# Optimization experiments

Hardware: AMD Instinct MI355X
Metric: run time of the kernel (lower is better)

The kernel has to match this reference:

```python
import jax, jax.numpy as jnp
import numpy as np

RATIO = 2
KSIZE = 12
PAD = KSIZE // 2 - RATIO // 2  # 5


def setup_inputs() -> dict:
    key = jax.random.key(0)
    k1, k2 = jax.random.split(key)
    x = jax.random.normal(k1, (4, 64, 256, 256), dtype=jnp.float32)
    # fixed anti-aliasing filter buffer (kaiser-jinc in original); random stand-in
    filt = jax.random.normal(k2, (KSIZE, KSIZE), dtype=jnp.float32)
    return {"x": x, "filt": filt}


def reference(x, filt):
    B, C, H, W = x.shape
    # reflect pad
    xp = jnp.pad(x, ((0, 0), (0, 0), (PAD, PAD), (PAD, PAD)), mode="reflect")
    # depthwise conv_transpose2d(stride=RATIO, groups=C) == conv with
    # lhs_dilation=RATIO, full padding (k-1), spatially flipped kernel
    w = jnp.broadcast_to(filt[::-1, ::-1][None, None], (C, 1, KSIZE, KSIZE))
    y = jax.lax.conv_general_dilated(
        xp, w,
        window_strides=(1, 1),
        padding=[(KSIZE - 1, KSIZE - 1)] * 2,
        lhs_dilation=(RATIO, RATIO),
        dimension_numbers=("NCHW", "OIHW", "NCHW"),
        feature_group_count=C,
    )
    y = (RATIO ** 2) * y
    pl = PAD * RATIO + (KSIZE - RATIO) // 2       # 15
    pr = PAD * RATIO + (KSIZE - RATIO + 1) // 2   # 15
    return y[..., pl:-pr, pl:-pr]
```

## Files before the change

### kernel.cpp

```cpp
#include <hip/hip_runtime.h>


#define S 40
#define TW 1552

typedef float v2f __attribute__((ext_vector_type(2)));
typedef __attribute__((address_space(3))) void lds_t;
typedef __attribute__((address_space(1))) const void gm_t;

__global__ void filter_prep(const float* __restrict__ filt, float* __restrict__ ws)
{
    int t = threadIdx.x;
    if (t < 144) {
        int n = t % 6, m = (t / 6) % 6, px = (t / 36) & 1, py = t / 72;
        float f = 4.0f * filt[(11 - py - 2 * m) * 12 + (11 - px - 2 * n)];
        ws[2 * t]     = f;
        ws[2 * t + 1] = f;
    }
}

__global__ __launch_bounds__(256, 4) void upsample2d_kernel(
    const float* __restrict__ x, const v2f* __restrict__ ftp,
    float* __restrict__ out)
{
    __shared__ float s_in[2 * TW];

    const int tx = threadIdx.x, ty = threadIdx.y;
    const int w    = ty >> 2;
    const int lane = (ty & 3) * 16 + tx;
    const int bc0 = blockIdx.z;
    const int boy = blockIdx.y, box = blockIdx.x;

    int goff[6];
    #pragma unroll
    for (int k = 0; k < 6; ++k) {
        int j = w * 384 + 64 * k + lane;
        if (j > 1519) j = 1519;
        int r = (j * 1639) >> 16;
        int c = j - r * 40;
        int gy = boy * 32 - 3 + r, gx = box * 32 - 3 + c;
        gy = gy < 0 ? -gy : gy;  gy = gy > 255 ? 510 - gy : gy;
        gx = gx < 0 ? -gx : gx;  gx = gx > 255 ? 510 - gx : gx;
        goff[k] = gy * 256 + gx;
    }

    const float* x0 = x + (size_t)bc0 * 65536;
    const float* x1 = x0 + (size_t)128 * 65536;

    #pragma unroll
    for (int k = 0; k < 6; ++k)
        __builtin_amdgcn_global_load_lds((gm_t*)(x0 + goff[k]),
                                         (lds_t*)(s_in + w * 384 + 64 * k), 4, 0, 0);
    #pragma unroll
    for (int k = 0; k < 6; ++k)
        __builtin_amdgcn_global_load_lds((gm_t*)(x1 + goff[k]),
                                         (lds_t*)(s_in + TW + w * 384 + 64 * k), 4, 0, 0);

    const int xb  = (2 * ty) * S + 2 * tx;
    const int OY0 = boy * 64 + 4 * ty;
    const int OX  = box * 64 + 4 * tx;

    auto tile = [&](const int sbase, float* oc) {
        v2f accp[4][2] = {};
        #pragma unroll
        for (int r = 0; r < 8; ++r) {
            const int rb = sbase + xb + r * S;
            v2f e[4], o[3];
            #pragma unroll
            for (int j = 0; j < 4; ++j)
                e[j] = *reinterpret_cast<const v2f*>(&s_in[rb + 2 * j]);
            #pragma unroll
            for (int j = 0; j < 3; ++j) {
                o[j].x = s_in[rb + 2 * j + 1];
                o[j].y = s_in[rb + 2 * j + 2];
            }
            #pragma unroll
            for (int qy = 0; qy < 2; ++qy)
            #pragma unroll
            for (int py = 0; py < 2; ++py) {
                const int m = r - qy - py;
                if (m >= 0 && m <= 5) {
                    #pragma unroll
                    for (int px = 0; px < 2; ++px)
                    #pragma unroll
                    for (int n = 0; n < 6; ++n) {
                        const int c = px + n;
                        const v2f xp = (c & 1) ? o[(c - 1) >> 1] : e[c >> 1];
                        const v2f f2 = ftp[((py * 2 + px) * 6 + m) * 6 + n];
                        accp[2 * qy + py][px] =
                            __builtin_elementwise_fma(xp, f2, accp[2 * qy + py][px]);
                    }
                }
            }
        }
        #pragma unroll
        for (int oy = 0; oy < 4; ++oy) {
            float4 v = make_float4(accp[oy][0].x, accp[oy][1].x,
                                   accp[oy][0].y, accp[oy][1].y);
            *reinterpret_cast<float4*>(&oc[(size_t)(OY0 + oy) * 512 + OX]) = v;
        }
    };

    asm volatile("s_waitcnt vmcnt(6)" ::: "memory");
    __builtin_amdgcn_sched_barrier(0);
    __builtin_amdgcn_s_barrier();
    __builtin_amdgcn_sched_barrier(0);
    tile(0, out + (size_t)bc0 * 262144);

    asm volatile("s_waitcnt vmcnt(16)" ::: "memory");
    __builtin_amdgcn_sched_barrier(0);
    __builtin_amdgcn_s_barrier();
    __builtin_amdgcn_sched_barrier(0);
    tile(TW, out + (size_t)(bc0 + 128) * 262144);
}

extern "C" void kernel_launch(void* const* d_in, const int* in_sizes, int n_in,
                              void* d_out, int out_size, void* d_ws, size_t ws_size,
                              hipStream_t stream) {
    const float* x    = (const float*)d_in[0];
    const float* filt = (const float*)d_in[1];
    float* out = (float*)d_out;
    float* ws  = (float*)d_ws;

    filter_prep<<<dim3(1), dim3(256), 0, stream>>>(filt, ws);

    dim3 grid(8, 8, 128);
    dim3 block(16, 16, 1);
    upsample2d_kernel<<<grid, block, 0, stream>>>(x, (const v2f*)ws, out);
}
```

Baseline: 85.03 us.

## Halve block size and compute two horizontal output groups per thread

The block shrinks to 128 threads, and each thread now produces 8 output columns instead of 4 for each of 4 rows. Each input row is read from LDS with two 128-bit loads and one 64-bit load, then the needed pairs are rebuilt with shuffles, so LDS reads and filter loads are shared across both column groups. Each thread issues twice as many async global-to-LDS loads, and the vmcnt wait counts are adjusted to match. This trades fewer waves per block and higher register pressure for better in-register reuse and fewer LDS instructions.

New measurement: 110.6 us. +30.1%, slower.

```diff
diff --git a/kernel.cpp b/kernel.cpp
--- a/kernel.cpp
+++ b/kernel.cpp
@@ -5,6 +5,7 @@
 #define TW 1552
 
 typedef float v2f __attribute__((ext_vector_type(2)));
+typedef float v4f __attribute__((ext_vector_type(4)));
 typedef __attribute__((address_space(3))) void lds_t;
 typedef __attribute__((address_space(1))) const void gm_t;
 
@@ -19,22 +20,22 @@
     }
 }
 
-__global__ __launch_bounds__(256, 4) void upsample2d_kernel(
+__global__ __launch_bounds__(128, 4) void upsample2d_kernel(
     const float* __restrict__ x, const v2f* __restrict__ ftp,
     float* __restrict__ out)
 {
-    __shared__ float s_in[2 * TW];
+    __shared__ alignas(16) float s_in[2 * TW];
 
     const int tx = threadIdx.x, ty = threadIdx.y;
-    const int w    = ty >> 2;
-    const int lane = (ty & 3) * 16 + tx;
+    const int w    = ty >> 3;
+    const int lane = tx + 8 * (ty & 7);
     const int bc0 = blockIdx.z;
     const int boy = blockIdx.y, box = blockIdx.x;
 
-    int goff[6];
+    int goff[12];
     #pragma unroll
-    for (int k = 0; k < 6; ++k) {
-        int j = w * 384 + 64 * k + lane;
+    for (int k = 0; k < 12; ++k) {
+        int j = w * 768 + 64 * k + lane;
         if (j > 1519) j = 1519;
         int r = (j * 1639) >> 16;
         int c = j - r * 40;
@@ -48,66 +49,74 @@
     const float* x1 = x0 + (size_t)128 * 65536;
 
     #pragma unroll
-    for (int k = 0; k < 6; ++k)
+    for (int k = 0; k < 12; ++k)
         __builtin_amdgcn_global_load_lds((gm_t*)(x0 + goff[k]),
-                                         (lds_t*)(s_in + w * 384 + 64 * k), 4, 0, 0);
+                                         (lds_t*)(s_in + w * 768 + 64 * k), 4, 0, 0);
     #pragma unroll
-    for (int k = 0; k < 6; ++k)
+    for (int k = 0; k < 12; ++k)
         __builtin_amdgcn_global_load_lds((gm_t*)(x1 + goff[k]),
-                                         (lds_t*)(s_in + TW + w * 384 + 64 * k), 4, 0, 0);
+                                         (lds_t*)(s_in + TW + w * 768 + 64 * k), 4, 0, 0);
 
-    const int xb  = (2 * ty) * S + 2 * tx;
     const int OY0 = boy * 64 + 4 * ty;
-    const int OX  = box * 64 + 4 * tx;
+    const int OX  = box * 64 + 8 * tx;
 
     auto tile = [&](const int sbase, float* oc) {
-        v2f accp[4][2] = {};
+        v2f accp[4][2][2] = {};
         #pragma unroll
         for (int r = 0; r < 8; ++r) {
-            const int rb = sbase + xb + r * S;
-            v2f e[4], o[3];
+            const int rb = sbase + (2 * ty + r) * S + 4 * tx;
+            v4f a  = *reinterpret_cast<const v4f*>(&s_in[rb]);
+            v4f b  = *reinterpret_cast<const v4f*>(&s_in[rb + 4]);
+            v2f c2 = *reinterpret_cast<const v2f*>(&s_in[rb + 8]);
+            v2f p[9];
+            p[0] = __builtin_shufflevector(a, a, 0, 1);
+            p[1] = __builtin_shufflevector(a, a, 1, 2);
+            p[2] = __builtin_shufflevector(a, a, 2, 3);
+            p[3] = __builtin_shufflevector(a, b, 3, 4);
+            p[4] = __builtin_shufflevector(b, b, 0, 1);
+            p[5] = __builtin_shufflevector(b, b, 1, 2);
+            p[6] = __builtin_shufflevector(b, b, 2, 3);
+            p[7] = (v2f){b.w, c2.x};
+            p[8] = c2;
             #pragma unroll
-            for (int j = 0; j < 4; ++j)
-                e[j] = *reinterpret_cast<const v2f*>(&s_in[rb + 2 * j]);
-            #pragma unroll
-            for (int j = 0; j < 3; ++j) {
-                o[j].x = s_in[rb + 2 * j + 1];
-                o[j].y = s_in[rb + 2 * j + 2];
-            }
-            #pragma unroll
-            for (int qy = 0; qy < 2; ++qy)
+            for (int yy = 0; yy < 2; ++yy)
             #pragma unroll
             for (int py = 0; py < 2; ++py) {
-                const int m = r - qy - py;
+                const int m = r - yy - py;
                 if (m >= 0 && m <= 5) {
                     #pragma unroll
                     for (int px = 0; px < 2; ++px)
                     #pragma unroll
                     for (int n = 0; n < 6; ++n) {
-                        const int c = px + n;
-                        const v2f xp = (c & 1) ? o[(c - 1) >> 1] : e[c >> 1];
                         const v2f f2 = ftp[((py * 2 + px) * 6 + m) * 6 + n];
-                        accp[2 * qy + py][px] =
-                            __builtin_elementwise_fma(xp, f2, accp[2 * qy + py][px]);
+                        #pragma unroll
+                        for (int j = 0; j < 2; ++j)
+                            accp[2 * yy + py][j][px] =
+                                __builtin_elementwise_fma(p[2 * j + px + n], f2,
+                                                          accp[2 * yy + py][j][px]);
                     }
                 }
             }
         }
         #pragma unroll
         for (int oy = 0; oy < 4; ++oy) {
-            float4 v = make_float4(accp[oy][0].x, accp[oy][1].x,
-                                   accp[oy][0].y, accp[oy][1].y);
-            *reinterpret_cast<float4*>(&oc[(size_t)(OY0 + oy) * 512 + OX]) = v;
+            float4 v0 = make_float4(accp[oy][0][0].x, accp[oy][0][1].x,
+                                    accp[oy][0][0].y, accp[oy][0][1].y);
+            float4 v1 = make_float4(accp[oy][1][0].x, accp[oy][1][1].x,
+                                    accp[oy][1][0].y, accp[oy][1][1].y);
+            float* row = &oc[(size_t)(OY0 + oy) * 512 + OX];
+            *reinterpret_cast<float4*>(row)     = v0;
+            *reinterpret_cast<float4*>(row + 4) = v1;
         }
     };
 
-    asm volatile("s_waitcnt vmcnt(6)" ::: "memory");
+    asm volatile("s_waitcnt vmcnt(12)" ::: "memory");
     __builtin_amdgcn_sched_barrier(0);
     __builtin_amdgcn_s_barrier();
     __builtin_amdgcn_sched_barrier(0);
     tile(0, out + (size_t)bc0 * 262144);
 
-    asm volatile("s_waitcnt vmcnt(16)" ::: "memory");
+    asm volatile("s_waitcnt vmcnt(8)" ::: "memory");
     __builtin_amdgcn_sched_barrier(0);
     __builtin_amdgcn_s_barrier();
     __builtin_amdgcn_sched_barrier(0);
@@ -125,6 +134,6 @@
     filter_prep<<<dim3(1), dim3(256), 0, stream>>>(filt, ws);
 
     dim3 grid(8, 8, 128);
-    dim3 block(16, 16, 1);
+    dim3 block(8, 16, 1);
     upsample2d_kernel<<<grid, block, 0, stream>>>(x, (const v2f*)ws, out);
 }
```
